# Kernel optimization log

Hardware: AMD Instinct MI355X
Metric: run time of the kernel (lower is better)

The kernel has to match this reference:

```python
import jax, jax.numpy as jnp
import numpy as np

B, P, S, E, H, NC, NR, NL = 32, 1024, 128, 768, 8, 5, 3, 3


def _adjacency():
    adj = np.zeros((NC, NC, NR), dtype=np.float32)
    for i, j in [(0, 1), (0, 2), (1, 2), (2, 3)]:  # co-occurrence (symmetric)
        adj[i, j, 0] = 1.0
        adj[j, i, 0] = 1.0
    adj[3, 2, 1] = 1.0  # hierarchical
    for i in range(NC):  # self loops
        adj[i, i, 2] = 1.0
    return jnp.asarray(adj)


def _ln(x, g, b, eps=1e-5):
    m = x.mean(-1, keepdims=True)
    v = ((x - m) ** 2).mean(-1, keepdims=True)
    return (x - m) * jax.lax.rsqrt(v + eps) * g + b


def _mha(q, k, v, Wqkv, bqkv, Wo, bo, h=H):
    # torch nn.MultiheadAttention, batch_first=True, eval mode (no dropout),
    # returns (output, attn weights averaged over heads)
    Bq, Lq, Eq = q.shape
    Lk = k.shape[1]
    d = Eq // h
    Wq, Wk, Wv = jnp.split(Wqkv, 3, axis=0)
    bq, bk, bv = jnp.split(bqkv, 3, axis=0)
    qh = (q @ Wq.T + bq).reshape(Bq, Lq, h, d).transpose(0, 2, 1, 3)
    kh = (k @ Wk.T + bk).reshape(Bq, Lk, h, d).transpose(0, 2, 1, 3)
    vh = (v @ Wv.T + bv).reshape(Bq, Lk, h, d).transpose(0, 2, 1, 3)
    scores = jnp.einsum('bhqd,bhkd->bhqk', qh, kh) / jnp.sqrt(jnp.asarray(d, q.dtype))
    a = jax.nn.softmax(scores, axis=-1)
    o = jnp.einsum('bhqk,bhkd->bhqd', a, vh).transpose(0, 2, 1, 3).reshape(Bq, Lq, Eq)
    return o @ Wo.T + bo, a.mean(axis=1)


def setup_inputs() -> dict:
    key = jax.random.key(0)
    ks = iter(jax.random.split(key, 64))
    n = lambda *s: jax.random.normal(next(ks), s, dtype=jnp.float32) * 0.02
    return {
        'visual_features': jax.random.normal(next(ks), (B, P, E), dtype=jnp.float32),
        'text_features': jax.random.normal(next(ks), (B, S, E), dtype=jnp.float32),
        'sentence_embedding': jax.random.normal(next(ks), (B, E), dtype=jnp.float32),
        'class_presence': (jax.random.uniform(next(ks), (B, NC)) > 0.5).astype(jnp.float32),
        # graph layer params stacked over NL layers
        'g_node_emb': n(NL, NC, E), 'g_edge_emb': n(NL, NR, E),
        'g_Wqkv': n(NL, 3 * E, E), 'g_bqkv': jnp.zeros((NL, 3 * E)),
        'g_Wo': n(NL, E, E), 'g_bo': jnp.zeros((NL, E)),
        'g_W1': n(NL, E, 2 * E), 'g_b1': jnp.zeros((NL, E)),
        'g_lng': jnp.ones((NL, E)), 'g_lnb': jnp.zeros((NL, E)),
        'g_W2': n(NL, E, E), 'g_b2': jnp.zeros((NL, E)),
        # visual-text fusion MHA
        'v_Wqkv': n(3 * E, E), 'v_bqkv': jnp.zeros((3 * E,)),
        'v_Wo': n(E, E), 'v_bo': jnp.zeros((E,)),
        # per-class feature generators stacked over NC classes
        'c_W1': n(NC, E, E), 'c_b1': jnp.zeros((NC, E)),
        'c_lng': jnp.ones((NC, E)), 'c_lnb': jnp.zeros((NC, E)),
        'c_W2': n(NC, E, E), 'c_b2': jnp.zeros((NC, E)),
        # global fusion MLP
        'gf_W1': n(E, 2 * E), 'gf_b1': jnp.zeros((E,)),
        'gf_lng': jnp.ones((E,)), 'gf_lnb': jnp.zeros((E,)),
        'gf_W2': n(E, E), 'gf_b2': jnp.zeros((E,)),
        # output proj + final norm
        'out_W': n(E, E), 'out_b': jnp.zeros((E,)),
        'norm_g': jnp.ones((E,)), 'norm_b': jnp.zeros((E,)),
    }


def reference(visual_features, text_features, sentence_embedding, class_presence,
              g_node_emb, g_edge_emb, g_Wqkv, g_bqkv, g_Wo, g_bo, g_W1, g_b1,
              g_lng, g_lnb, g_W2, g_b2, v_Wqkv, v_bqkv, v_Wo, v_bo,
              c_W1, c_b1, c_lng, c_lnb, c_W2, c_b2,
              gf_W1, gf_b1, gf_lng, gf_lnb, gf_W2, gf_b2,
              out_W, out_b, norm_g, norm_b):
    adj = _adjacency()
    Bc = visual_features.shape[0]
    sent = sentence_embedding
    activated, scores = None, None
    for l in range(NL):  # small fixed layer loop
        node_emb = g_node_emb[l]  # [NC, E]
        # sum over relation types of (adj_r @ node_emb) * edge_emb_r, / NR
        edge_feat = jnp.einsum('ijr,je,re->ie', adj, node_emb, g_edge_emb[l]) / NR
        node_f = jnp.broadcast_to(node_emb, (Bc, NC, E))
        combined = jnp.concatenate([node_f, jnp.broadcast_to(edge_feat, (Bc, NC, E))], axis=-1)
        h = combined @ g_W1[l].T + g_b1[l]
        h = jax.nn.relu(_ln(h, g_lng[l], g_lnb[l]))
        updated = h @ g_W2[l].T + g_b2[l]  # [B, NC, E]
        _, w = _mha(sent[:, None, :], updated, updated, g_Wqkv[l], g_bqkv[l], g_Wo[l], g_bo[l])
        scores = jax.nn.softmax(w[:, 0, :] * (class_presence + 0.1), axis=-1)
        activated = updated * scores[..., None]
        sent = sent + activated.mean(axis=1)
    fused, _ = _mha(visual_features, text_features, text_features, v_Wqkv, v_bqkv, v_Wo, v_bo)
    grounded = _ln(visual_features + fused, norm_g, norm_b)
    # grouped per-class MLPs (batched over classes via einsum)
    cf = jnp.einsum('bce,cfe->bcf', activated, c_W1) + c_b1
    cf = jax.nn.relu(_ln(cf, c_lng, c_lnb))
    cf = jnp.einsum('bce,cfe->bcf', cf, c_W2) + c_b2
    gc = jnp.broadcast_to(sent[:, None, :], (Bc, NC, E))
    g = jnp.concatenate([cf, gc], axis=-1) @ gf_W1.T + gf_b1
    g = jax.nn.relu(_ln(g, gf_lng, gf_lnb))
    class_guidance = g @ gf_W2.T + gf_b2
    grounded_out = grounded @ out_W.T + out_b
    return grounded_out, class_guidance, scores
```

## Files before the change

### kernel.cpp

```cpp
#include <hip/hip_runtime.h>
#include <stdint.h>

typedef unsigned short u16;
typedef __attribute__((ext_vector_type(8))) short short8;
typedef __attribute__((ext_vector_type(4))) float f32x4;

#define NB 32
#define PP 1024
#define SEQ 128
#define EE 768
#define HH 8
#define DD 96
#define NCC 5
#define NLL 3

__device__ __forceinline__ float bf2f(u16 x){ unsigned u=((unsigned)x)<<16; float f; __builtin_memcpy(&f,&u,4); return f; }
__device__ __forceinline__ u16 f2bf(float f){ unsigned u; __builtin_memcpy(&u,&f,4); u=(u+0x7FFFu+((u>>16)&1u))>>16; return (u16)u; }

__device__ __forceinline__ short8 cvt8(const float* p) {
  f32x4 a = *(const f32x4*)p;
  f32x4 b = *(const f32x4*)(p+4);
  short8 r;
  r[0]=(short)f2bf(a[0]); r[1]=(short)f2bf(a[1]); r[2]=(short)f2bf(a[2]); r[3]=(short)f2bf(a[3]);
  r[4]=(short)f2bf(b[0]); r[5]=(short)f2bf(b[1]); r[6]=(short)f2bf(b[2]); r[7]=(short)f2bf(b[3]);
  return r;
}

__device__ __forceinline__ void gl16(const u16* g, u16* l) {
  __builtin_amdgcn_global_load_lds((const __attribute__((address_space(1))) void*)g,
                                   (__attribute__((address_space(3))) void*)l, 16, 0, 0);
}

__global__ __launch_bounds__(256) void k_cvt4(
    const float* __restrict__ s0, u16* __restrict__ d0, int c0,
    const float* __restrict__ s1, u16* __restrict__ d1, int c1,
    const float* __restrict__ s2, u16* __restrict__ d2, int c2,
    const float* __restrict__ s3, u16* __restrict__ d3, int c3)
{
  int i = blockIdx.x*256 + threadIdx.x;
  const int stride = gridDim.x*256;
  const int tot = c0+c1+c2+c3;
  for (; i < tot; i += stride) {
    int j = i; const float* s; u16* d;
    if (j < c0) { s=s0; d=d0; }
    else { j-=c0; if (j<c1){s=s1;d=d1;}
      else { j-=c1; if (j<c2){s=s2;d=d2;} else { j-=c2; s=s3; d=d3; } } }
    *(short8*)(d + (size_t)j*8) = cvt8(s + (size_t)j*8);
  }
}

__global__ __launch_bounds__(256) void k_cvt(const float* __restrict__ s, u16* __restrict__ d, int n8) {
  int i = blockIdx.x*256 + threadIdx.x;
  const int stride = gridDim.x*256;
  for (; i < n8; i += stride) *(short8*)(d + (size_t)i*8) = cvt8(s + (size_t)i*8);
}

__device__ __forceinline__ void ln_stats(float v0, float v1, float v2, float* red, int t,
                                         float& mean, float& rstd) {
  float ps = v0+v1+v2;
  float ps2 = v0*v0+v1*v1+v2*v2;
  #pragma unroll
  for (int o=32;o;o>>=1){ ps += __shfl_down(ps,o,64); ps2 += __shfl_down(ps2,o,64); }
  if ((t&63)==0){ red[t>>6]=ps; red[4+(t>>6)]=ps2; }
  __syncthreads();
  mean = (red[0]+red[1]+red[2]+red[3])*(1.0f/EE);
  float var = (red[4]+red[5]+red[6]+red[7])*(1.0f/EE) - mean*mean;
  rstd = rsqrtf(var + 1e-5f);
  __syncthreads();
}

template<int EPI>
__global__ __launch_bounds__(256) void gemm_bt(const u16* __restrict__ A, const u16* __restrict__ Bw,
        const float* __restrict__ bias, const u16* __restrict__ Res,
        u16* __restrict__ C, float* __restrict__ Cf, u16* __restrict__ C2,
        int M, int N, int K, int NTB)
{
  __shared__ u16 As[2][4096];
  __shared__ u16 Bs[2][4096];
  const int nwg = gridDim.x;
  const int bid = blockIdx.x;
  const int task = (bid & 7)*(nwg >> 3) + (bid >> 3);
  const int m0 = (task / NTB)*128, n0 = (task % NTB)*128;
  const int t = threadIdx.x;
  const int lane = t&63, w = t>>6, wr = w>>1, wc = w&1, lm = lane&15, lg = lane>>4;
  const int o   = w*1024 + lane*16;
  const int srow = o>>6;
  const int sg   = ((o>>4)&3) ^ ((srow>>1)&3);
  const u16* ag = A  + (size_t)(m0+srow)*K + sg*8;
  const u16* bg = Bw + (size_t)(n0+srow)*K + sg*8;
  const size_t rstep = (size_t)64*K;
  const int s  = (lm>>1)&3;
  const int ra = (wr*64+lm)*32 + (lg^s)*8;
  const int rb = (wc*64+lm)*32 + (lg^s)*8;

  f32x4 acc[4][4] = {};
  gl16(ag,         &As[0][w*512]);
  gl16(ag + rstep, &As[0][2048 + w*512]);
  gl16(bg,         &Bs[0][w*512]);
  gl16(bg + rstep, &Bs[0][2048 + w*512]);
  __syncthreads();
  int cur = 0;
  const int NT = K>>5;
  for (int kt=0; kt<NT; ++kt) {
    if (kt+1 < NT) {
      const int k0 = (kt+1)<<5;
      gl16(ag + k0,         &As[cur^1][w*512]);
      gl16(ag + k0 + rstep, &As[cur^1][2048 + w*512]);
      gl16(bg + k0,         &Bs[cur^1][w*512]);
      gl16(bg + k0 + rstep, &Bs[cur^1][2048 + w*512]);
    }
    short8 af[4], bf[4];
    #pragma unroll
    for (int mi=0;mi<4;mi++) af[mi] = *(const short8*)&As[cur][ra + mi*512];
    #pragma unroll
    for (int ni=0;ni<4;ni++) bf[ni] = *(const short8*)&Bs[cur][rb + ni*512];
    #pragma unroll
    for (int mi=0;mi<4;mi++)
      #pragma unroll
      for (int ni=0;ni<4;ni++)
        acc[mi][ni] = __builtin_amdgcn_mfma_f32_16x16x32_bf16(af[mi], bf[ni], acc[mi][ni], 0,0,0);
    __syncthreads();
    cur ^= 1;
  }
  #pragma unroll
  for (int mi=0;mi<4;mi++) {
    #pragma unroll
    for (int ni=0;ni<4;ni++) {
      const int col = n0 + wc*64 + ni*16 + lm;
      const float bv = bias[col];
      #pragma unroll
      for (int r=0;r<4;r++) {
        const int row = m0 + wr*64 + mi*16 + lg*4 + r;
        float v = acc[mi][ni][r] + bv;
        if constexpr (EPI==1) v += bf2f(Res[(size_t)row*N + col]);
        if constexpr (EPI==3) {
          Cf[(size_t)row*N + col] = v;
        } else if constexpr (EPI==2) {
          if (col < EE) C[(size_t)row*EE + col] = f2bf(v);
          else C2[((size_t)(row>>7)*EE + (col-EE))*SEQ + (row&127)] = f2bf(v);
        } else {
          C[(size_t)row*N + col] = f2bf(v);
        }
      }
    }
  }
}

template<int MT, int AF>
__global__ __launch_bounds__(256) void gemm_tk(const void* __restrict__ Av, const float* __restrict__ W,
    float* __restrict__ Ppart, int ngroups, int KS, int K, int lda, long strideA, long strideW)
{
  const int task = blockIdx.x;
  const int nt = task % 6;
  const int g  = (task/6) % ngroups;
  const int ks = task/(6*ngroups);
  const int t = threadIdx.x, l = t&63, w = t>>6, lm = l&15, lg = l>>4;
  const int slice = K/KS, kbase = ks*slice;
  const int n0 = nt*128 + w*32;
  W += (size_t)g*strideW;
  f32x4 acc[MT/16][2] = {};
  for (int ki=0; ki<slice; ki+=32) {
    const int k0 = kbase + ki;
    short8 af[MT/16];
    #pragma unroll
    for (int m=0;m<MT/16;m++) {
      if constexpr (AF) af[m] = cvt8((const float*)Av + (size_t)g*strideA + (size_t)(m*16+lm)*lda + k0 + lg*8);
      else af[m] = *(const short8*)((const u16*)Av + (size_t)g*strideA + (size_t)(m*16+lm)*lda + k0 + lg*8);
    }
    #pragma unroll
    for (int ni=0;ni<2;ni++) {
      const short8 bf = cvt8(W + (size_t)(n0+ni*16+lm)*K + k0 + lg*8);
      #pragma unroll
      for (int m=0;m<MT/16;m++)
        acc[m][ni] = __builtin_amdgcn_mfma_f32_16x16x32_bf16(af[m], bf, acc[m][ni], 0,0,0);
    }
  }
  float* pb = Ppart + (size_t)(ks*ngroups+g)*MT*768;
  #pragma unroll
  for (int m=0;m<MT/16;m++)
    #pragma unroll
    for (int ni=0;ni<2;ni++)
      #pragma unroll
      for (int r=0;r<4;r++)
        pb[(size_t)(m*16+lg*4+r)*768 + n0+ni*16+lm] = acc[m][ni][r];
}

__global__ __launch_bounds__(256) void k_red(const float* __restrict__ Ppart,
    float* __restrict__ outF, u16* __restrict__ outB,
    const float* __restrict__ bias, long strideB,
    int MT, int ngroups, int KS, int Mreal, long strideR, long strideG)
{
  const int bid = blockIdx.x, g = bid/Mreal, rr = bid%Mreal, t = threadIdx.x;
  #pragma unroll
  for (int i=0;i<3;i++) {
    const int e = t + i*256;
    float s = bias[(size_t)g*strideB + e];
    for (int ks=0; ks<KS; ++ks) s += Ppart[((size_t)(ks*ngroups+g)*MT + rr)*768 + e];
    const size_t off = (size_t)rr*strideR + (size_t)g*strideG + e;
    if (outF) outF[off] = s;
    if (outB) outB[off] = f2bf(s);
  }
}

__global__ __launch_bounds__(256) void k_lnred(const float* __restrict__ Ppart, u16* __restrict__ out,
    const float* __restrict__ bias, long strideB,
    const float* __restrict__ gamma, const float* __restrict__ beta, long strideLn,
    int MT, int ngroups, int KS, int Mreal, long strideR, long strideG)
{
  const int bid = blockIdx.x, g = bid/Mreal, rr = bid%Mreal, t = threadIdx.x;
  __shared__ float red[8];
  float v[3];
  #pragma unroll
  for (int i=0;i<3;i++) {
    const int e = t + i*256;
    float s = bias[(size_t)g*strideB + e];
    for (int ks=0; ks<KS; ++ks) s += Ppart[((size_t)(ks*ngroups+g)*MT + rr)*768 + e];
    v[i] = s;
  }
  float mean, rstd;
  ln_stats(v[0],v[1],v[2], red, t, mean, rstd);
  #pragma unroll
  for (int i=0;i<3;i++) {
    const int e = t + i*256;
    out[(size_t)rr*strideR + (size_t)g*strideG + e] =
        f2bf(fmaxf((v[i]-mean)*rstd*gamma[(size_t)g*strideLn+e]+beta[(size_t)g*strideLn+e], 0.f));
  }
}

__global__ __launch_bounds__(256) void k_comb_si(const float* __restrict__ node_all,
    const float* __restrict__ edge_all, u16* __restrict__ comb,
    const float* __restrict__ se, float* __restrict__ sent)
{
  const int bid = blockIdx.x, t = threadIdx.x;
  if (bid < NLL*NCC) {
    const int ll = bid/NCC, c = bid%NCC;
    const float* node = node_all + (size_t)ll*NCC*EE;
    const float* edge = edge_all + (size_t)ll*3*EE;
    #pragma unroll
    for (int i=0;i<3;i++) {
      const int e = t + i*256;
      float n0=node[e], n1=node[EE+e], n2=node[2*EE+e], n3=node[3*EE+e];
      float nc_=node[(size_t)c*EE+e];
      float e0=edge[e], e1=edge[EE+e], e2=edge[2*EE+e];
      float s0;
      if (c==0) s0=n1+n2; else if (c==1) s0=n0+n2; else if (c==2) s0=n0+n1+n3; else if (c==3) s0=n2; else s0=0.f;
      float ef = (s0*e0 + ((c==3)? n2*e1 : 0.f) + nc_*e2)*(1.0f/3.0f);
      comb[(size_t)bid*2*EE + e]      = f2bf(nc_);
      comb[(size_t)bid*2*EE + EE + e] = f2bf(ef);
    }
  } else {
    const int i = (bid - NLL*NCC)*256 + t;
    if (i < NB*EE) sent[i] = se[i];
  }
}

__global__ __launch_bounds__(256) void k_attn2(int l, const float* __restrict__ qpart,
    const float* __restrict__ bq,
    const float* __restrict__ presence, const float* __restrict__ upd, const float* __restrict__ khg,
    float* __restrict__ sent, float* __restrict__ sc_ws, float* __restrict__ out_scores,
    u16* __restrict__ actB, u16* __restrict__ cat)
{
  const int b = blockIdx.x, t = threadIdx.x;
  __shared__ float qh[EE];
  __shared__ float scl[HH][NCC];
  __shared__ float wsc[NCC];
  __shared__ float scr[NCC];
  #pragma unroll
  for (int i=0;i<3;i++) {
    const int e = t + i*256;
    float s = bq[e];
    #pragma unroll
    for (int ks=0; ks<8; ++ks) s += qpart[((size_t)ks*NB + b)*768 + e];
    qh[e] = s;
  }
  __syncthreads();
  if (t < HH*NCC) {
    const int hh=t/NCC, cc=t%NCC;
    const float* kr = khg + (size_t)(l*NCC+cc)*EE + hh*DD;
    float a=0.f;
    #pragma unroll 8
    for (int d=0;d<DD;d++) a += qh[hh*DD+d]*kr[d];
    scl[hh][cc]=a*0.1020620726159658f;
  }
  __syncthreads();
  if (t < HH) {
    float m=scl[t][0];
    #pragma unroll
    for (int c2=1;c2<NCC;c2++) m=fmaxf(m,scl[t][c2]);
    float ex[NCC]; float s=0.f;
    #pragma unroll
    for (int c2=0;c2<NCC;c2++){ ex[c2]=__expf(scl[t][c2]-m); s+=ex[c2]; }
    #pragma unroll
    for (int c2=0;c2<NCC;c2++) scl[t][c2]=ex[c2]/s;
  }
  __syncthreads();
  if (t < NCC) {
    float wv=0.f;
    #pragma unroll
    for (int hh=0;hh<HH;hh++) wv += scl[hh][t];
    wv *= (1.0f/HH);
    wsc[t] = wv*(presence[b*NCC+t]+0.1f);
  }
  __syncthreads();
  if (t==0) {
    float m=wsc[0];
    #pragma unroll
    for (int c2=1;c2<NCC;c2++) m=fmaxf(m,wsc[c2]);
    float ex[NCC]; float s=0.f;
    #pragma unroll
    for (int c2=0;c2<NCC;c2++){ ex[c2]=__expf(wsc[c2]-m); s+=ex[c2]; }
    #pragma unroll
    for (int c2=0;c2<NCC;c2++){
      float v=ex[c2]/s; scr[c2]=v; sc_ws[b*NCC+c2]=v;
      if (out_scores) out_scores[b*NCC+c2]=v;
    }
  }
  __syncthreads();
  #pragma unroll
  for (int i=0;i<3;i++) {
    const int e=t+i*256;
    float a=0.f;
    #pragma unroll
    for (int c2=0;c2<NCC;c2++) a += scr[c2]*upd[(size_t)(l*NCC+c2)*EE+e];
    const float sn = sent[(size_t)b*EE+e] + a*(1.0f/NCC);
    sent[(size_t)b*EE+e] = sn;
    if (out_scores) {
      const u16 snb = f2bf(sn);
      #pragma unroll
      for (int c2=0;c2<NCC;c2++) {
        actB[((size_t)c2*NB + b)*EE + e] = f2bf(upd[(size_t)(2*NCC+c2)*EE + e]*scr[c2]);
        cat[((size_t)(b*NCC+c2))*2*EE + EE + e] = snb;
      }
    }
  }
}

__global__ __launch_bounds__(256) void attn_k(u16* __restrict__ Q, const u16* __restrict__ Kb,
                                              const u16* __restrict__ Vt)
{
  const int qt = blockIdx.x, h = blockIdx.y, b = blockIdx.z;
  const int t = threadIdx.x, l = t&63, w = t>>6, wr = w>>1, wc = w&1, lm = l&15, lg = l>>4;
  __shared__ u16 Ps[64][136];
  __shared__ float redm[2][64];
  __shared__ float reds[2][64];
  u16* qb = Q + ((size_t)(b*PP + qt*64))*EE + h*DD;
  const u16* kb = Kb + ((size_t)b*SEQ)*EE + h*DD;
  const u16* vb = Vt + ((size_t)(b*HH+h))*DD*SEQ;

  f32x4 acc[2][4] = {};
  #pragma unroll
  for (int kc=0;kc<3;kc++) {
    short8 af[2], bv[4];
    #pragma unroll
    for (int mi=0;mi<2;mi++) af[mi] = *(const short8*)(qb + (size_t)(wr*32+mi*16+lm)*EE + kc*32 + lg*8);
    #pragma unroll
    for (int ni=0;ni<4;ni++) bv[ni] = *(const short8*)(kb + (size_t)(wc*64+ni*16+lm)*EE + kc*32 + lg*8);
    #pragma unroll
    for (int mi=0;mi<2;mi++)
      #pragma unroll
      for (int ni=0;ni<4;ni++)
        acc[mi][ni] = __builtin_amdgcn_mfma_f32_16x16x32_bf16(af[mi], bv[ni], acc[mi][ni], 0,0,0);
  }
  const float scale = 0.1020620726159658f;
  float gmax[2][4], gsum[2][4];
  #pragma unroll
  for (int mi=0;mi<2;mi++)
    #pragma unroll
    for (int r=0;r<4;r++) {
      float v = fmaxf(fmaxf(acc[mi][0][r],acc[mi][1][r]),fmaxf(acc[mi][2][r],acc[mi][3][r]));
      #pragma unroll
      for (int mk=1;mk<16;mk<<=1) v = fmaxf(v, __shfl_xor(v,mk,64));
      gmax[mi][r]=v;
    }
  if (lm==0) {
    #pragma unroll
    for (int mi=0;mi<2;mi++)
      #pragma unroll
      for (int r=0;r<4;r++) redm[wc][wr*32+mi*16+lg*4+r] = gmax[mi][r];
  }
  __syncthreads();
  #pragma unroll
  for (int mi=0;mi<2;mi++)
    #pragma unroll
    for (int r=0;r<4;r++) {
      const int row = wr*32+mi*16+lg*4+r;
      gmax[mi][r] = fmaxf(redm[0][row], redm[1][row]);
    }
  #pragma unroll
  for (int mi=0;mi<2;mi++)
    #pragma unroll
    for (int r=0;r<4;r++) {
      float s=0.f;
      #pragma unroll
      for (int ni=0;ni<4;ni++) {
        float p = __expf((acc[mi][ni][r]-gmax[mi][r])*scale);
        acc[mi][ni][r]=p; s+=p;
      }
      #pragma unroll
      for (int mk=1;mk<16;mk<<=1) s += __shfl_xor(s,mk,64);
      gsum[mi][r]=s;
    }
  __syncthreads();
  if (lm==0) {
    #pragma unroll
    for (int mi=0;mi<2;mi++)
      #pragma unroll
      for (int r=0;r<4;r++) reds[wc][wr*32+mi*16+lg*4+r] = gsum[mi][r];
  }
  __syncthreads();
  #pragma unroll
  for (int mi=0;mi<2;mi++)
    #pragma unroll
    for (int r=0;r<4;r++) {
      const int row = wr*32+mi*16+lg*4+r;
      const float inv = 1.0f/(reds[0][row]+reds[1][row]);
      #pragma unroll
      for (int ni=0;ni<4;ni++)
        Ps[row][wc*64+ni*16+lm] = f2bf(acc[mi][ni][r]*inv);
    }
  __syncthreads();

  f32x4 oacc[2][3] = {};
  #pragma unroll
  for (int kc=0;kc<4;kc++) {
    short8 pa[2], vv[3];
    #pragma unroll
    for (int mi=0;mi<2;mi++) pa[mi] = *(const short8*)&Ps[wr*32+mi*16+lm][kc*32+lg*8];
    #pragma unroll
    for (int ni=0;ni<3;ni++) vv[ni] = *(const short8*)(vb + (size_t)(wc*48+ni*16+lm)*SEQ + kc*32 + lg*8);
    #pragma unroll
    for (int mi=0;mi<2;mi++)
      #pragma unroll
      for (int ni=0;ni<3;ni++)
        oacc[mi][ni] = __builtin_amdgcn_mfma_f32_16x16x32_bf16(pa[mi], vv[ni], oacc[mi][ni], 0,0,0);
  }
  #pragma unroll
  for (int mi=0;mi<2;mi++)
    #pragma unroll
    for (int ni=0;ni<3;ni++)
      #pragma unroll
      for (int r=0;r<4;r++)
        qb[(size_t)(wr*32+mi*16+lg*4+r)*EE + wc*48+ni*16+lm] = f2bf(oacc[mi][ni][r]);
}

__global__ __launch_bounds__(256) void k_ln(u16* __restrict__ G, const float* __restrict__ gw, const float* __restrict__ gb)
{
  const int row = blockIdx.x, t = threadIdx.x;
  u16* p = G + (size_t)row*EE;
  __shared__ float red[8];
  float v[3];
  #pragma unroll
  for (int i=0;i<3;i++) v[i]=bf2f(p[t+i*256]);
  float mean, rstd;
  ln_stats(v[0],v[1],v[2], red, t, mean, rstd);
  #pragma unroll
  for (int i=0;i<3;i++) {
    const int e=t+i*256;
    p[e]=f2bf((v[i]-mean)*rstd*gw[e]+gb[e]);
  }
}

extern "C" void kernel_launch(void* const* d_in, const int* in_sizes, int n_in,
                              void* d_out, int out_size, void* d_ws, size_t ws_size,
                              hipStream_t stream)
{
  const float* visual   = (const float*)d_in[0];
  const float* text     = (const float*)d_in[1];
  const float* sentemb  = (const float*)d_in[2];
  const float* presence = (const float*)d_in[3];
  const float* gnode = (const float*)d_in[4];
  const float* gedge = (const float*)d_in[5];
  const float* gWqkv = (const float*)d_in[6];
  const float* gbqkv = (const float*)d_in[7];
  const float* gW1 = (const float*)d_in[10];
  const float* gb1 = (const float*)d_in[11];
  const float* glng = (const float*)d_in[12];
  const float* glnb = (const float*)d_in[13];
  const float* gW2 = (const float*)d_in[14];
  const float* gb2 = (const float*)d_in[15];
  const float* vWqkv = (const float*)d_in[16];
  const float* vbqkv = (const float*)d_in[17];
  const float* vWo = (const float*)d_in[18];
  const float* vbo = (const float*)d_in[19];
  const float* cW1 = (const float*)d_in[20];
  const float* cb1 = (const float*)d_in[21];
  const float* clng = (const float*)d_in[22];
  const float* clnb = (const float*)d_in[23];
  const float* cW2 = (const float*)d_in[24];
  const float* cb2 = (const float*)d_in[25];
  const float* gfW1 = (const float*)d_in[26];
  const float* gfb1 = (const float*)d_in[27];
  const float* gflng = (const float*)d_in[28];
  const float* gflnb = (const float*)d_in[29];
  const float* gfW2 = (const float*)d_in[30];
  const float* gfb2 = (const float*)d_in[31];
  const float* outW = (const float*)d_in[32];
  const float* outb = (const float*)d_in[33];
  const float* normg = (const float*)d_in[34];
  const float* normb = (const float*)d_in[35];

  char* ws = (char*)d_ws;
  u16* wsG   = (u16*)(ws);
  u16* wsK   = (u16*)(ws + 50331648);
  u16* wsVt  = (u16*)(ws + 56623104);
  u16* visB  = (u16*)(ws + 62914560);
  u16* outWB = wsK;

  char* dob = (char*)d_out;
  u16* wsQ    = (u16*)(dob);
  u16* textB  = (u16*)(dob + 50331648);
  u16* WqkvB  = (u16*)(dob + 56623104);
  u16* WoB    = (u16*)(dob + 60162048);
  char* P = dob + 61341696;
  float* wsSent   = (float*)(P);
  float* wsUpd    = (float*)(P +   98304);
  float* wsKhg    = (float*)(P +  144384);
  float* wsScores = (float*)(P +  190464);
  u16*   wsComb   = (u16*)  (P +  191104);
  u16*   wsHb     = (u16*)  (P +  237184);
  u16*   wsUpdB   = (u16*)  (P +  260224);
  u16*   wsActB   = (u16*)  (P +  283264);
  u16*   wsH1b    = (u16*)  (P +  529024);
  u16*   wsCat    = (u16*)  (P +  774784);
  u16*   wsG1b    = (u16*)  (P + 1266304);
  float* Ppart    = (float*)(P + 1512064);

  float* outGO = (float*)d_out;
  float* outCG = outGO + 25165824;
  float* outSC = outGO + 25288704;

  k_cvt4<<<dim3(2048), dim3(256), 0, stream>>>(visual, visB, 3145728,
                                               text, textB, 393216,
                                               vWqkv, WqkvB, 221184,
                                               vWo, WoB, 73728);

  k_comb_si<<<dim3(NLL*NCC + 96), dim3(256), 0, stream>>>(gnode, gedge, wsComb, sentemb, wsSent);
  gemm_tk<16,0><<<dim3(144), dim3(256), 0, stream>>>(wsComb, gW1, Ppart,
      3, 8, 2*EE, 2*EE, (long)NCC*2*EE, (long)EE*2*EE);
  k_lnred<<<dim3(15), dim3(256), 0, stream>>>(Ppart, wsHb, gb1, EE, glng, glnb, EE,
      16, 3, 8, 5, 768, 3840);
  gemm_tk<16,0><<<dim3(72), dim3(256), 0, stream>>>(wsHb, gW2, Ppart,
      3, 4, EE, EE, (long)NCC*EE, (long)EE*EE);
  k_red<<<dim3(15), dim3(256), 0, stream>>>(Ppart, wsUpd, wsUpdB, gb2, EE,
      16, 3, 4, 5, 768, 3840);
  gemm_tk<16,0><<<dim3(72), dim3(256), 0, stream>>>(wsUpdB, gWqkv + (size_t)EE*EE, Ppart,
      3, 4, EE, EE, (long)NCC*EE, (long)3*EE*EE);
  k_red<<<dim3(15), dim3(256), 0, stream>>>(Ppart, wsKhg, nullptr, gbqkv + EE, (long)3*EE,
      16, 3, 4, 5, 768, 3840);

  for (int l=0;l<NLL;l++) {
    gemm_tk<32,1><<<dim3(48), dim3(256), 0, stream>>>(wsSent, gWqkv + (size_t)l*3*EE*EE, Ppart,
        1, 8, EE, EE, 0, 0);
    k_attn2<<<dim3(NB), dim3(256), 0, stream>>>(l, Ppart, gbqkv + (size_t)l*3*EE,
        presence, wsUpd, wsKhg, wsSent, wsScores,
        (l==NLL-1)?outSC:(float*)nullptr, wsActB, wsCat);
  }

  gemm_tk<32,0><<<dim3(120), dim3(256), 0, stream>>>(wsActB, cW1, Ppart,
      5, 4, EE, EE, (long)NB*EE, (long)EE*EE);
  k_lnred<<<dim3(160), dim3(256), 0, stream>>>(Ppart, wsH1b, cb1, EE, clng, clnb, EE,
      32, 5, 4, 32, 768, 24576);
  gemm_tk<32,0><<<dim3(120), dim3(256), 0, stream>>>(wsH1b, cW2, Ppart,
      5, 4, EE, EE, (long)NB*EE, (long)EE*EE);
  k_red<<<dim3(160), dim3(256), 0, stream>>>(Ppart, nullptr, wsCat, cb2, EE,
      32, 5, 4, 32, 7680, 1536);
  gemm_tk<32,0><<<dim3(120), dim3(256), 0, stream>>>(wsCat, gfW1, Ppart,
      5, 4, 2*EE, 2*EE, (long)NB*2*EE, 0);
  k_lnred<<<dim3(160), dim3(256), 0, stream>>>(Ppart, wsG1b, gfb1, 0, gflng, gflnb, 0,
      32, 5, 4, 32, 768, 24576);
  gemm_tk<32,0><<<dim3(120), dim3(256), 0, stream>>>(wsG1b, gfW2, Ppart,
      5, 4, EE, EE, (long)NB*EE, 0);
  k_red<<<dim3(160), dim3(256), 0, stream>>>(Ppart, outCG, nullptr, gfb2, 0,
      32, 5, 4, 32, 768, 24576);

  gemm_bt<0><<<dim3(1536), dim3(256), 0, stream>>>(visB, WqkvB, vbqkv, nullptr,
                                                   wsQ, nullptr, nullptr, NB*PP, EE, EE, 6);
  gemm_bt<2><<<dim3(384), dim3(256), 0, stream>>>(textB, WqkvB + (size_t)EE*EE, vbqkv+EE, nullptr,
                                                  wsK, nullptr, wsVt, NB*SEQ, 2*EE, EE, 12);
  attn_k<<<dim3(PP/64, HH, NB), dim3(256), 0, stream>>>(wsQ, wsK, wsVt);
  k_cvt<<<dim3(512), dim3(256), 0, stream>>>(outW, outWB, 73728);
  gemm_bt<1><<<dim3(1536), dim3(256), 0, stream>>>(wsQ, WoB, vbo, visB,
                                                   wsG, nullptr, nullptr, NB*PP, EE, EE, 6);
  k_ln<<<dim3(NB*PP), dim3(256), 0, stream>>>(wsG, normg, normb);
  gemm_bt<3><<<dim3(1536), dim3(256), 0, stream>>>(wsG, outWB, outb, nullptr,
                                                   nullptr, outGO, nullptr, NB*PP, EE, EE, 6);
}
```

Before: 474.7 us.

## Triple-buffer GEMM LDS tiles with explicit vmcnt waits and prefetch distance two

Moves the bf16 GEMM main loop from double to triple buffering in shared memory. Loads run two tiles ahead, and synchronisation uses explicit s_waitcnt vmcnt counts plus raw barriers instead of __syncthreads. After fragments are read into registers, a second barrier frees the current buffer so the next load can be issued before the MFMAs. The aim is to hide global-load latency behind more compute. The cost is 1.5x the LDS footprint (48KB per block), which may reduce occupancy, and correctness depends on the hand-coded vmcnt values matching the gl16 instruction count.

After: 460.0 us. 1.03x faster.

```diff
diff --git a/kernel.cpp b/kernel.cpp
--- a/kernel.cpp
+++ b/kernel.cpp
@@ -75,8 +75,8 @@
         u16* __restrict__ C, float* __restrict__ Cf, u16* __restrict__ C2,
         int M, int N, int K, int NTB)
 {
-  __shared__ u16 As[2][4096];
-  __shared__ u16 Bs[2][4096];
+  __shared__ u16 As[3][4096];
+  __shared__ u16 Bs[3][4096];
   const int nwg = gridDim.x;
   const int bid = blockIdx.x;
   const int task = (bid & 7)*(nwg >> 3) + (bid >> 3);
@@ -92,35 +92,45 @@
   const int s  = (lm>>1)&3;
   const int ra = (wr*64+lm)*32 + (lg^s)*8;
   const int rb = (wc*64+lm)*32 + (lg^s)*8;
+  const int NT = K>>5;
 
   f32x4 acc[4][4] = {};
-  gl16(ag,         &As[0][w*512]);
-  gl16(ag + rstep, &As[0][2048 + w*512]);
-  gl16(bg,         &Bs[0][w*512]);
-  gl16(bg + rstep, &Bs[0][2048 + w*512]);
-  __syncthreads();
+  #pragma unroll
+  for (int p=0;p<3;p++) {
+    const int k0 = p<<5;
+    gl16(ag + k0,         &As[p][w*512]);
+    gl16(ag + k0 + rstep, &As[p][2048 + w*512]);
+    gl16(bg + k0,         &Bs[p][w*512]);
+    gl16(bg + k0 + rstep, &Bs[p][2048 + w*512]);
+  }
   int cur = 0;
-  const int NT = K>>5;
   for (int kt=0; kt<NT; ++kt) {
-    if (kt+1 < NT) {
-      const int k0 = (kt+1)<<5;
-      gl16(ag + k0,         &As[cur^1][w*512]);
-      gl16(ag + k0 + rstep, &As[cur^1][2048 + w*512]);
-      gl16(bg + k0,         &Bs[cur^1][w*512]);
-      gl16(bg + k0 + rstep, &Bs[cur^1][2048 + w*512]);
-    }
+    if (kt+2 < NT)      { asm volatile("s_waitcnt vmcnt(8)" ::: "memory"); }
+    else if (kt+1 < NT) { asm volatile("s_waitcnt vmcnt(4)" ::: "memory"); }
+    else                { asm volatile("s_waitcnt vmcnt(0)" ::: "memory"); }
+    __builtin_amdgcn_sched_barrier(0);
+    __builtin_amdgcn_s_barrier();
     short8 af[4], bf[4];
     #pragma unroll
     for (int mi=0;mi<4;mi++) af[mi] = *(const short8*)&As[cur][ra + mi*512];
     #pragma unroll
     for (int ni=0;ni<4;ni++) bf[ni] = *(const short8*)&Bs[cur][rb + ni*512];
+    asm volatile("s_waitcnt lgkmcnt(0)" ::: "memory");
+    __builtin_amdgcn_sched_barrier(0);
+    __builtin_amdgcn_s_barrier();
+    if (kt+3 < NT) {
+      const int k0 = (kt+3)<<5;
+      gl16(ag + k0,         &As[cur][w*512]);
+      gl16(ag + k0 + rstep, &As[cur][2048 + w*512]);
+      gl16(bg + k0,         &Bs[cur][w*512]);
+      gl16(bg + k0 + rstep, &Bs[cur][2048 + w*512]);
+    }
     #pragma unroll
     for (int mi=0;mi<4;mi++)
       #pragma unroll
       for (int ni=0;ni<4;ni++)
         acc[mi][ni] = __builtin_amdgcn_mfma_f32_16x16x32_bf16(af[mi], bf[ni], acc[mi][ni], 0,0,0);
-    __syncthreads();
-    cur ^= 1;
+    cur = (cur==2) ? 0 : cur+1;
   }
   #pragma unroll
   for (int mi=0;mi<4;mi++) {
```
